# Kernel optimization log

Measured on AMD Instinct MI355X. Metric: run time of the kernel, lower is better.

The kernel has to match this reference:

```python
import jax, jax.numpy as jnp
import numpy as np


def setup_inputs() -> dict:
    key = jax.random.key(0)
    k1, k2 = jax.random.split(key)
    x = jax.random.normal(k1, (32, 128, 56, 56), dtype=jnp.float32)
    weight = jax.random.normal(k2, (256, 128, 3, 3), dtype=jnp.float32) * 0.01
    bias = jnp.zeros((256,), dtype=jnp.float32)
    return {"x": x, "weight": weight, "bias": bias}


def reference(x, weight, bias):
    # Faithful to Conv2dGEMM: im2col + GEMM is mathematically a standard
    # cross-correlation conv with the given stride/padding. We express it as
    # the efficient fused form (implicit GEMM) which computes identical math.
    stride, padding = 1, 1
    out = jax.lax.conv_general_dilated(
        x, weight,
        window_strides=(stride, stride),
        padding=[(padding, padding), (padding, padding)],
        dimension_numbers=("NCHW", "OIHW", "NCHW"),
    )  # [B, out_ch, H_out, W_out]
    return out + bias[None, :, None, None]
```

## Files before the change

kernel.cpp:

```cpp
#include <hip/hip_runtime.h>
#include <stdint.h>

typedef __bf16 bf16x8 __attribute__((ext_vector_type(8)));
typedef float  f32x4  __attribute__((ext_vector_type(4)));

#define NB   32
#define CI   128
#define HH   56
#define WW   56
#define CO   256
#define HP   58
#define HW   (HH*WW)
#define MTOT (NB*HW)
#define KTOT 1152

#define XT_ELEMS ((size_t)NB*HP*HP*CI)
#define XT_BYTES (XT_ELEMS*2)

#define XPOSE_BLKS 1792
#define WX_BLKS    1152
#define HALO_BLKS  456
__global__ void prep_kernel(const float* __restrict__ x, const float* __restrict__ wg,
                            __bf16* __restrict__ xt, __bf16* __restrict__ wt) {
  __shared__ float tile[CI][57];
  int bid = blockIdx.x;
  int t = threadIdx.x;
  if (bid < XPOSE_BLKS) {
    int n = bid / HH, h = bid % HH;
    const float* src = x + (size_t)n * CI * HW + (size_t)h * WW;
    for (int idx = t; idx < CI * 14; idx += 256) {
      int c = idx / 14, w4 = idx - c * 14;
      float4 v = *(const float4*)(src + (size_t)c * HW + w4 * 4);
      tile[c][w4 * 4 + 0] = v.x;
      tile[c][w4 * 4 + 1] = v.y;
      tile[c][w4 * 4 + 2] = v.z;
      tile[c][w4 * 4 + 3] = v.w;
    }
    __syncthreads();
    __bf16* dst = xt + ((size_t)(n * HP + h + 1) * HP + 1) * CI;
    for (int idx = t; idx < WW * 16; idx += 256) {
      int w = idx >> 4, c8 = (idx & 15) * 8;
      bf16x8 v;
      for (int k = 0; k < 8; ++k) v[k] = (__bf16)tile[c8 + k][w];
      *(bf16x8*)(dst + (size_t)w * CI + c8) = v;
    }
  } else if (bid < XPOSE_BLKS + WX_BLKS) {
    int id = (bid - XPOSE_BLKS) * 256 + t;
    int o = id / KTOT;
    int k = id - o * KTOT;
    int rs = k >> 7, c = k & 127;
    wt[id] = (__bf16)wg[(size_t)o * KTOT + c * 9 + rs];
  } else {
    int id = (bid - XPOSE_BLKS - WX_BLKS) * 256 + t;
    if (id < NB * 228 * 16) {
      int chunk = id & 15;
      int p = (id >> 4) % 228;
      int n = id / (228 * 16);
      int h, w;
      if (p < 58)       { h = 0;           w = p; }
      else if (p < 116) { h = 57;          w = p - 58; }
      else if (p < 172) { h = p - 116 + 1; w = 0; }
      else              { h = p - 172 + 1; w = 57; }
      int4* dst = (int4*)(xt + ((size_t)(n * HP + h) * HP + w) * CI) + chunk;
      *dst = make_int4(0, 0, 0, 0);
    }
  }
}

#define BM 128
#define BN 128
#define NKIT 36

__device__ __forceinline__ void gload_lds16(const __bf16* g, __bf16* l) {
  __builtin_amdgcn_global_load_lds(
      (const __attribute__((address_space(1))) void*)g,
      (__attribute__((address_space(3))) void*)l, 16, 0, 0);
}

__global__ __launch_bounds__(256, 3) void conv_gemm(
    const __bf16* __restrict__ xt, const __bf16* __restrict__ wt,
    const float* __restrict__ bias, float* __restrict__ out) {
  __shared__ __bf16 Alds[2][BM * 32];
  __shared__ __bf16 Blds[2][BN * 32];
  int t = threadIdx.x;
  int bx = blockIdx.x;
  int nb = bx & 1, mb = bx >> 1;

  size_t baseA[2], baseB[2];
  __bf16* ldsA[2][2];
  __bf16* ldsB[2][2];
  for (int i = 0; i < 2; ++i) {
    int ml = i * 64 + (t >> 2);
    unsigned m = mb * BM + ml;
    unsigned nimg = m / HW;
    unsigned hw = m - nimg * HW;
    unsigned h = hw / WW;
    unsigned w = hw - h * WW;
    baseA[i] = ((size_t)(nimg * HP + h) * HP + w) * CI + (t & 3) * 8;
    baseB[i] = (size_t)(nb * BN + ml) * KTOT + (t & 3) * 8;
    for (int p = 0; p < 2; ++p) {
      ldsA[i][p] = &Alds[p][ml * 32 + (t & 3) * 8];
      ldsB[i][p] = &Blds[p][ml * 32 + (t & 3) * 8];
    }
  }

  int wid = t >> 6, lane = t & 63;
  int wm = (wid >> 1) * 64, wn = (wid & 1) * 64;
  int lr = lane & 15, lk = (lane >> 4) * 8;

  f32x4 acc[4][4];
  for (int i = 0; i < 4; ++i)
    for (int j = 0; j < 4; ++j) acc[i][j] = (f32x4){0.f, 0.f, 0.f, 0.f};

  gload_lds16(xt + baseA[0], ldsA[0][0]);
  gload_lds16(xt + baseA[1], ldsA[1][0]);
  gload_lds16(wt + baseB[0], ldsB[0][0]);
  gload_lds16(wt + baseB[1], ldsB[1][0]);

#pragma unroll 2
  for (int kt = 0; kt < NKIT; ++kt) {
    int cur = kt & 1;
    __syncthreads();
    if (kt != NKIT - 1) {
      int kn = kt + 1;
      int rs = kn >> 2;
      int r = (rs * 11) >> 5;
      int s = rs - 3 * r;
      size_t offA = ((size_t)(r * HP + s)) * CI + (size_t)(kn & 3) * 32;
      size_t offB = (size_t)kn * 32;
      int nxt = cur ^ 1;
      gload_lds16(xt + baseA[0] + offA, ldsA[0][nxt]);
      gload_lds16(xt + baseA[1] + offA, ldsA[1][nxt]);
      gload_lds16(wt + baseB[0] + offB, ldsB[0][nxt]);
      gload_lds16(wt + baseB[1] + offB, ldsB[1][nxt]);
    }
    bf16x8 a[4], b[4];
    for (int i = 0; i < 4; ++i) {
      a[i] = *(const bf16x8*)&Alds[cur][(wm + i * 16 + lr) * 32 + lk];
      b[i] = *(const bf16x8*)&Blds[cur][(wn + i * 16 + lr) * 32 + lk];
    }
    for (int i = 0; i < 4; ++i)
      for (int j = 0; j < 4; ++j)
        acc[i][j] = __builtin_amdgcn_mfma_f32_16x16x32_bf16(a[i], b[j], acc[i][j], 0, 0, 0);
  }

  for (int j = 0; j < 4; ++j) {
    int o = nb * BN + wn + j * 16 + lr;
    float bv = bias[o];
    for (int i = 0; i < 4; ++i) {
      unsigned m0 = mb * BM + wm + i * 16 + (lane >> 4) * 4;
      unsigned nimg = m0 / HW;
      unsigned hw = m0 - nimg * HW;
      f32x4 v = acc[i][j] + bv;
      *(f32x4*)(out + ((size_t)nimg * CO + o) * HW + hw) = v;
    }
  }
}

extern "C" void kernel_launch(void* const* d_in, const int* in_sizes, int n_in,
                              void* d_out, int out_size, void* d_ws, size_t ws_size,
                              hipStream_t stream) {
  const float* x    = (const float*)d_in[0];
  const float* wg   = (const float*)d_in[1];
  const float* bias = (const float*)d_in[2];
  float* out = (float*)d_out;

  __bf16* xt = (__bf16*)d_ws;
  __bf16* wt = (__bf16*)((char*)d_ws + XT_BYTES);

  prep_kernel<<<XPOSE_BLKS + WX_BLKS + HALO_BLKS, 256, 0, stream>>>(x, wg, xt, wt);
  conv_gemm<<<(MTOT / BM) * (CO / BN), 256, 0, stream>>>(xt, wt, bias, out);
}
```

Baseline: 229.3 us.

## Load weights pre-swizzled into MFMA fragment order straight from global memory, stage full-tap A tiles

The prep kernel now writes the bf16 weights in MFMA fragment order, so each lane reads its B operand directly from global memory (through cache) and B no longer goes through LDS. The A tile grows to all 128 channels of one filter tap, stored with an XOR swizzle to avoid bank conflicts. The K loop now has 9 iterations instead of 36, which cuts barriers and address arithmetic. The double buffering is removed, so global-to-LDS loads no longer overlap MFMA work. LDS use stays at 32KB per block, and the per-lane global B loads may add latency.

```diff
diff --git a/kernel.cpp b/kernel.cpp
--- a/kernel.cpp
+++ b/kernel.cpp
@@ -21,7 +21,7 @@
 #define WX_BLKS    1152
 #define HALO_BLKS  456
 __global__ void prep_kernel(const float* __restrict__ x, const float* __restrict__ wg,
-                            __bf16* __restrict__ xt, __bf16* __restrict__ wt) {
+                            __bf16* __restrict__ xt, __bf16* __restrict__ wts) {
   __shared__ float tile[CI][57];
   int bid = blockIdx.x;
   int t = threadIdx.x;
@@ -46,10 +46,14 @@
     }
   } else if (bid < XPOSE_BLKS + WX_BLKS) {
     int id = (bid - XPOSE_BLKS) * 256 + t;
-    int o = id / KTOT;
-    int k = id - o * KTOT;
+    int e   = id & 7;
+    int ln  = (id >> 3) & 63;
+    int n16 = (id >> 9) & 15;
+    int kc  = id >> 13;
+    int o = n16 * 16 + (ln & 15);
+    int k = kc * 32 + (ln >> 4) * 8 + e;
     int rs = k >> 7, c = k & 127;
-    wt[id] = (__bf16)wg[(size_t)o * KTOT + c * 9 + rs];
+    wts[id] = (__bf16)wg[(size_t)o * KTOT + c * 9 + rs];
   } else {
     int id = (bid - XPOSE_BLKS - WX_BLKS) * 256 + t;
     if (id < NB * 228 * 16) {
@@ -68,8 +72,6 @@
 }
 
 #define BM 128
-#define BN 128
-#define NKIT 36
 
 __device__ __forceinline__ void gload_lds16(const __bf16* g, __bf16* l) {
   __builtin_amdgcn_global_load_lds(
@@ -78,77 +80,66 @@
 }
 
 __global__ __launch_bounds__(256, 3) void conv_gemm(
-    const __bf16* __restrict__ xt, const __bf16* __restrict__ wt,
+    const __bf16* __restrict__ xt, const __bf16* __restrict__ wts,
     const float* __restrict__ bias, float* __restrict__ out) {
-  __shared__ __bf16 Alds[2][BM * 32];
-  __shared__ __bf16 Blds[2][BN * 32];
+  __shared__ __bf16 Alds[BM * 128];
   int t = threadIdx.x;
   int bx = blockIdx.x;
   int nb = bx & 1, mb = bx >> 1;
 
-  size_t baseA[2], baseB[2];
-  __bf16* ldsA[2][2];
-  __bf16* ldsB[2][2];
-  for (int i = 0; i < 2; ++i) {
-    int ml = i * 64 + (t >> 2);
-    unsigned m = mb * BM + ml;
+  unsigned k8s = (t & 15) ^ (t >> 4);
+  unsigned rowOff[8];
+  for (int r = 0; r < 8; ++r) {
+    unsigned m = mb * BM + r * 16 + (t >> 4);
     unsigned nimg = m / HW;
     unsigned hw = m - nimg * HW;
     unsigned h = hw / WW;
     unsigned w = hw - h * WW;
-    baseA[i] = ((size_t)(nimg * HP + h) * HP + w) * CI + (t & 3) * 8;
-    baseB[i] = (size_t)(nb * BN + ml) * KTOT + (t & 3) * 8;
-    for (int p = 0; p < 2; ++p) {
-      ldsA[i][p] = &Alds[p][ml * 32 + (t & 3) * 8];
-      ldsB[i][p] = &Blds[p][ml * 32 + (t & 3) * 8];
-    }
+    rowOff[r] = ((nimg * HP + h) * HP + w) * CI + k8s * 8;
   }
 
   int wid = t >> 6, lane = t & 63;
   int wm = (wid >> 1) * 64, wn = (wid & 1) * 64;
-  int lr = lane & 15, lk = (lane >> 4) * 8;
+  int lr = lane & 15, lhi = lane >> 4;
+  unsigned n16base = (unsigned)(nb * 128 + wn) >> 4;
+  const bf16x8* wfrag = (const bf16x8*)wts;
 
   f32x4 acc[4][4];
   for (int i = 0; i < 4; ++i)
     for (int j = 0; j < 4; ++j) acc[i][j] = (f32x4){0.f, 0.f, 0.f, 0.f};
 
-  gload_lds16(xt + baseA[0], ldsA[0][0]);
-  gload_lds16(xt + baseA[1], ldsA[1][0]);
-  gload_lds16(wt + baseB[0], ldsB[0][0]);
-  gload_lds16(wt + baseB[1], ldsB[1][0]);
-
-#pragma unroll 2
-  for (int kt = 0; kt < NKIT; ++kt) {
-    int cur = kt & 1;
+  for (int kt = 0; kt < 9; ++kt) {
+    int r = (kt * 11) >> 5;
+    int s = kt - 3 * r;
+    unsigned tapOff = (unsigned)(r * HP + s) * CI;
+    if (kt) __syncthreads();
+#pragma unroll
+    for (int rr = 0; rr < 8; ++rr)
+      gload_lds16(xt + rowOff[rr] + tapOff, &Alds[rr * 2048 + t * 8]);
     __syncthreads();
-    if (kt != NKIT - 1) {
-      int kn = kt + 1;
-      int rs = kn >> 2;
-      int r = (rs * 11) >> 5;
-      int s = rs - 3 * r;
-      size_t offA = ((size_t)(r * HP + s)) * CI + (size_t)(kn & 3) * 32;
-      size_t offB = (size_t)kn * 32;
-      int nxt = cur ^ 1;
-      gload_lds16(xt + baseA[0] + offA, ldsA[0][nxt]);
-      gload_lds16(xt + baseA[1] + offA, ldsA[1][nxt]);
-      gload_lds16(wt + baseB[0] + offB, ldsB[0][nxt]);
-      gload_lds16(wt + baseB[1] + offB, ldsB[1][nxt]);
+#pragma unroll
+    for (int subk = 0; subk < 4; ++subk) {
+      unsigned kc = (unsigned)kt * 4 + subk;
+      bf16x8 b[4];
+      for (int j = 0; j < 4; ++j)
+        b[j] = wfrag[(kc * 16 + n16base + j) * 64 + lane];
+      bf16x8 a[4];
+      for (int i = 0; i < 4; ++i) {
+        unsigned m = wm + i * 16 + lr;
+        unsigned phys = m * 16 + ((subk * 4 + lhi) ^ lr);
+        a[i] = *(const bf16x8*)&Alds[phys * 8];
+      }
+      for (int i = 0; i < 4; ++i)
+        for (int j = 0; j < 4; ++j)
+          acc[i][j] = __builtin_amdgcn_mfma_f32_16x16x32_bf16(a[i], b[j], acc[i][j], 0, 0, 0);
     }
-    bf16x8 a[4], b[4];
-    for (int i = 0; i < 4; ++i) {
-      a[i] = *(const bf16x8*)&Alds[cur][(wm + i * 16 + lr) * 32 + lk];
-      b[i] = *(const bf16x8*)&Blds[cur][(wn + i * 16 + lr) * 32 + lk];
-    }
-    for (int i = 0; i < 4; ++i)
-      for (int j = 0; j < 4; ++j)
-        acc[i][j] = __builtin_amdgcn_mfma_f32_16x16x32_bf16(a[i], b[j], acc[i][j], 0, 0, 0);
   }
 
   for (int j = 0; j < 4; ++j) {
-    int o = nb * BN + wn + j * 16 + lr;
+    int o = nb * 128 + wn + j * 16 + lr;
     float bv = bias[o];
     for (int i = 0; i < 4; ++i) {
-      unsigned m0 = mb * BM + wm + i * 16 + (lane >> 4) * 4;
+      unsigned m0 = mb * BM + wm + i * 16 + lhi * 4;
       unsigned nimg = m0 / HW;
       unsigned hw = m0 - nimg * HW;
       f32x4 v = acc[i][j] + bv;
@@ -165,9 +156,9 @@
   const float* bias = (const float*)d_in[2];
   float* out = (float*)d_out;
 
-  __bf16* xt = (__bf16*)d_ws;
-  __bf16* wt = (__bf16*)((char*)d_ws + XT_BYTES);
+  __bf16* xt  = (__bf16*)d_ws;
+  __bf16* wts = (__bf16*)((char*)d_ws + XT_BYTES);
 
-  prep_kernel<<<XPOSE_BLKS + WX_BLKS + HALO_BLKS, 256, 0, stream>>>(x, wg, xt, wt);
-  conv_gemm<<<(MTOT / BM) * (CO / BN), 256, 0, stream>>>(xt, wt, bias, out);
+  prep_kernel<<<XPOSE_BLKS + WX_BLKS + HALO_BLKS, 256, 0, stream>>>(x, wg, xt, wts);
+  conv_gemm<<<(MTOT / BM) * (CO / 128), 256, 0, stream>>>(xt, wts, bias, out);
 }
```

After: 225.2 us. Within noise of the previous version (-1.8%).
